# Kernel tuning notes

Measured on AMD Instinct MI355X. Metric: run time of the kernel, lower is better.

Reference implementation:

```python
import jax, jax.numpy as jnp
import numpy as np

B, T, D, M = 4, 4096, 2048, 512


def setup_inputs() -> dict:
    key = jax.random.key(0)
    ks = jax.random.split(key, 6)
    x = jax.random.normal(ks[0], (B, T, D), dtype=jnp.float32)
    memory_state = jnp.zeros((B, M), dtype=jnp.float32)
    # xavier_normal-style init for the linear layers, zero biases
    Wv = jax.random.normal(ks[1], (M, D), dtype=jnp.float32) * np.float32(np.sqrt(2.0 / (D + M)))
    bv = jnp.zeros((M,), dtype=jnp.float32)
    Wg = jax.random.normal(ks[2], (D, D + M), dtype=jnp.float32) * np.float32(np.sqrt(2.0 / (2 * D + M)))
    bg = jnp.zeros((D,), dtype=jnp.float32)
    time_decay = jax.random.normal(ks[3], (M,), dtype=jnp.float32) * 0.01
    time_first = jax.random.normal(ks[4], (M,), dtype=jnp.float32) * 0.01
    return dict(x=x, memory_state=memory_state, Wv=Wv, bv=bv, Wg=Wg, bg=bg,
                time_decay=time_decay, time_first=time_first)


def reference(x, memory_state, Wv, bv, Wg, bg, time_decay, time_first):
    # v = value_proj(x): [B, T, M]
    v = jnp.einsum('btd,md->btm', x, Wv) + bv
    decay = jax.nn.sigmoid(time_decay) * 0.9 + 0.1   # [M]
    first = jax.nn.sigmoid(time_first)               # [M]

    # Recurrence: s_0 = memory_state; wv_t = v_t + s_t*first; s_{t+1} = s_t*decay + v_t
    def step(s, v_t):
        wv_t = v_t + s * first
        return s * decay + v_t, wv_t

    v_tb = jnp.swapaxes(v, 0, 1)                     # [T, B, M] for scan over time
    next_memory, wv_tb = jax.lax.scan(step, memory_state, v_tb)
    weighted_values = jnp.swapaxes(wv_tb, 0, 1)      # [B, T, M]

    # output = x + output_gate(concat[x, weighted_values])
    combined = jnp.concatenate([x, weighted_values], axis=-1)  # [B, T, D+M]
    output = x + jnp.einsum('btk,dk->btd', combined, Wg) + bg
    return output, next_memory
```

## Files before the change

### kernel.cpp

```cpp
#include <hip/hip_runtime.h>
#include <hip/hip_bf16.h>
#include <stdint.h>

#define BB 4
#define TT 4096
#define DDIM 2048
#define MDIM 512
#define NROWS (BB * TT)
#define KCAT (DDIM + MDIM)
#define CHUNK 64
#define NCH (TT / CHUNK)

typedef __attribute__((ext_vector_type(8))) short bf16x8;
typedef __attribute__((ext_vector_type(4))) float f32x4;

#define WAITVM(N) asm volatile("s_waitcnt vmcnt(" #N ")" ::: "memory")
#define SBAR()    asm volatile("s_barrier" ::: "memory")

__device__ __forceinline__ unsigned short f2bf(float f) {
  unsigned u = __float_as_uint(f);
  return (unsigned short)((u + 0x7fffu + ((u >> 16) & 1u)) >> 16);
}
__device__ __forceinline__ float sigm(float x) { return 1.0f / (1.0f + expf(-x)); }

__device__ __forceinline__ void gload16(const void* g, void* l) {
  __builtin_amdgcn_global_load_lds(
      (const __attribute__((address_space(1))) unsigned int*)g,
      (__attribute__((address_space(3))) unsigned int*)l, 16, 0, 0);
}

__global__ void cvt_x_kernel(const float* __restrict__ x, unsigned short* __restrict__ comb) {
  size_t i = (size_t)blockIdx.x * 256 + threadIdx.x;
  size_t row = i >> 9;
  size_t c = (i & 511) << 2;
  float4 f = ((const float4*)x)[i];
  ushort4 o;
  o.x = f2bf(f.x); o.y = f2bf(f.y); o.z = f2bf(f.z); o.w = f2bf(f.w);
  *((ushort4*)(comb + row * KCAT + c)) = o;
}

__global__ void cvt_w_kernel(const float* __restrict__ src, unsigned short* __restrict__ dst, long n4) {
  long i = (long)blockIdx.x * 256 + threadIdx.x;
  if (i >= n4) return;
  float4 f = ((const float4*)src)[i];
  ushort4 o;
  o.x = f2bf(f.x); o.y = f2bf(f.y); o.z = f2bf(f.z); o.w = f2bf(f.w);
  ((ushort4*)dst)[i] = o;
}

template<int EPI>
__global__ __launch_bounds__(256, 3) void gemm_bf16_kernel(
    const unsigned short* __restrict__ A, long lda,
    const unsigned short* __restrict__ B, long K,
    float* __restrict__ out, long ldo,
    const float* __restrict__ bias,
    const float* __restrict__ xres,
    int ncb)
{
  __shared__ __align__(16) unsigned char ldsA[3][8192];
  __shared__ __align__(16) unsigned char ldsB[3][8192];

  const int tid = threadIdx.x;
  const int nwg = gridDim.x;
  int lin = blockIdx.x;
  lin = (lin & 7) * (nwg >> 3) + (lin >> 3);
  const long row0 = (long)(lin / ncb) * 128;
  const long col0 = (long)(lin % ncb) * 128;

  const int lane = tid & 63;
  const int wave = tid >> 6;
  const int wr = (wave >> 1) * 64;
  const int wc = (wave & 1) * 64;

  const int srow = tid >> 2;
  const int skq = ((tid & 3) ^ ((tid >> 3) & 3)) * 8;
  const unsigned short* aS = A + (row0 + srow) * lda + skq;
  const unsigned short* bS = B + (col0 + srow) * K + skq;
  const int ldst = tid * 16;

  f32x4 acc[4][4];
#pragma unroll
  for (int i = 0; i < 4; ++i)
#pragma unroll
    for (int j = 0; j < 4; ++j)
      acc[i][j] = {0.f, 0.f, 0.f, 0.f};

  int aOff[4], bOff[4];
#pragma unroll
  for (int i = 0; i < 4; ++i) {
    const int ra = wr + i * 16 + (lane & 15);
    const int rb = wc + i * 16 + (lane & 15);
    aOff[i] = ra * 64 + ((((lane >> 4) ^ ((ra >> 1) & 3))) << 4);
    bOff[i] = rb * 64 + ((((lane >> 4) ^ ((rb >> 1) & 3))) << 4);
  }

  const int nt = (int)(K >> 5);

  auto STAGE = [&](int buf, int t) {
    const long koff = (long)t << 5;
#pragma unroll
    for (int j = 0; j < 2; ++j) {
      gload16(aS + koff + (long)j * 64 * lda, &ldsA[buf][j * 4096 + ldst]);
      gload16(bS + koff + (long)j * 64 * K, &ldsB[buf][j * 4096 + ldst]);
    }
  };

  auto COMPUTE = [&](int cb) {
    bf16x8 af[4], bfr[4];
#pragma unroll
    for (int i = 0; i < 4; ++i) af[i] = *(const bf16x8*)(&ldsA[cb][aOff[i]]);
#pragma unroll
    for (int i = 0; i < 4; ++i) bfr[i] = *(const bf16x8*)(&ldsB[cb][bOff[i]]);
    __builtin_amdgcn_s_setprio(1);
#pragma unroll
    for (int i = 0; i < 4; ++i)
#pragma unroll
      for (int j = 0; j < 4; ++j)
        acc[i][j] = __builtin_amdgcn_mfma_f32_16x16x32_bf16(af[i], bfr[j], acc[i][j], 0, 0, 0);
    __builtin_amdgcn_s_setprio(0);
  };

  STAGE(0, 0);
  STAGE(1, 1);
  int cur = 0, stg = 2;
  for (int t = 0; t < nt - 2; ++t) {
    WAITVM(4);
    SBAR();
    STAGE(stg, t + 2);
    COMPUTE(cur);
    cur = (cur == 2) ? 0 : cur + 1;
    stg = (stg == 2) ? 0 : stg + 1;
  }
  WAITVM(4);
  SBAR();
  COMPUTE(cur);
  cur = (cur == 2) ? 0 : cur + 1;
  WAITVM(0);
  SBAR();
  COMPUTE(cur);

  const int orow = (lane >> 4) * 4;
  const int ocol = lane & 15;
#pragma unroll
  for (int i = 0; i < 4; ++i) {
    const long gr0 = row0 + wr + i * 16 + orow;
#pragma unroll
    for (int j = 0; j < 4; ++j) {
      const long gc = col0 + wc + j * 16 + ocol;
      const float bb = bias[gc];
#pragma unroll
      for (int r = 0; r < 4; ++r) {
        const long gr = gr0 + r;
        float v = acc[i][j][r] + bb;
        if (EPI == 1) v += xres[gr * ldo + gc];
        out[gr * ldo + gc] = v;
      }
    }
  }
}

__global__ void scan_local_kernel(const float* __restrict__ v, float* __restrict__ s_loc,
                                  const float* __restrict__ td) {
  const int m = threadIdx.x;
  const int c = blockIdx.x;
  const int b = blockIdx.y;
  const float decay = sigm(td[m]) * 0.9f + 0.1f;
  const float* vp = v + ((size_t)b * TT + (size_t)c * CHUNK) * MDIM + m;
  float s = 0.f;
#pragma unroll 8
  for (int t = 0; t < CHUNK; ++t) s = s * decay + vp[(size_t)t * MDIM];
  s_loc[((size_t)b * NCH + c) * MDIM + m] = s;
}

__global__ void scan_chunks_kernel(const float* __restrict__ s_loc, const float* __restrict__ mem0,
                                   float* __restrict__ s_in, float* __restrict__ nextmem,
                                   const float* __restrict__ td) {
  const int m = threadIdx.x;
  const int b = blockIdx.x;
  const float decay = sigm(td[m]) * 0.9f + 0.1f;
  const float d2 = decay * decay, d4 = d2 * d2, d8 = d4 * d4;
  const float d16 = d8 * d8, d32 = d16 * d16, dL = d32 * d32;
  float s = mem0[(size_t)b * MDIM + m];
  for (int c = 0; c < NCH; ++c) {
    const size_t idx = ((size_t)b * NCH + c) * MDIM + m;
    s_in[idx] = s;
    s = s * dL + s_loc[idx];
  }
  nextmem[(size_t)b * MDIM + m] = s;
}

__global__ void scan_replay_kernel(const float* __restrict__ v, const float* __restrict__ s_in,
                                   unsigned short* __restrict__ comb,
                                   const float* __restrict__ td, const float* __restrict__ tf) {
  const int m = threadIdx.x;
  const int c = blockIdx.x;
  const int b = blockIdx.y;
  const float decay = sigm(td[m]) * 0.9f + 0.1f;
  const float first = sigm(tf[m]);
  float s = s_in[((size_t)b * NCH + c) * MDIM + m];
  const float* vp = v + ((size_t)b * TT + (size_t)c * CHUNK) * MDIM + m;
  unsigned short* wp = comb + ((size_t)b * TT + (size_t)c * CHUNK) * KCAT + DDIM + m;
#pragma unroll 4
  for (int t = 0; t < CHUNK; ++t) {
    const float vv = vp[(size_t)t * MDIM];
    wp[(size_t)t * KCAT] = f2bf(vv + s * first);
    s = s * decay + vv;
  }
}

extern "C" void kernel_launch(void* const* d_in, const int* in_sizes, int n_in,
                              void* d_out, int out_size, void* d_ws, size_t ws_size,
                              hipStream_t stream) {
  const float* x    = (const float*)d_in[0];
  const float* mem0 = (const float*)d_in[1];
  const float* Wv   = (const float*)d_in[2];
  const float* bv   = (const float*)d_in[3];
  const float* Wg   = (const float*)d_in[4];
  const float* bg   = (const float*)d_in[5];
  const float* td   = (const float*)d_in[6];
  const float* tf   = (const float*)d_in[7];

  float* out = (float*)d_out;
  float* nextmem = out + (size_t)NROWS * DDIM;
  float* vbuf = out;

  unsigned short* comb = (unsigned short*)d_ws;
  unsigned short* WvB  = comb + (size_t)NROWS * KCAT;
  unsigned short* WgB  = WvB + (size_t)MDIM * DDIM;
  float* s_loc = (float*)(WgB + (size_t)DDIM * KCAT);
  float* s_in  = s_loc + (size_t)BB * NCH * MDIM;

  cvt_x_kernel<<<(NROWS * DDIM / 4) / 256, 256, 0, stream>>>(x, comb);
  cvt_w_kernel<<<(MDIM * DDIM / 4) / 256, 256, 0, stream>>>(Wv, WvB, (long)MDIM * DDIM / 4);
  cvt_w_kernel<<<(DDIM * KCAT / 4) / 256, 256, 0, stream>>>(Wg, WgB, (long)DDIM * KCAT / 4);

  gemm_bf16_kernel<0><<<(NROWS / 128) * (MDIM / 128), 256, 0, stream>>>(
      comb, KCAT, WvB, DDIM, vbuf, MDIM, bv, nullptr, MDIM / 128);

  scan_local_kernel<<<dim3(NCH, BB), MDIM, 0, stream>>>(vbuf, s_loc, td);
  scan_chunks_kernel<<<BB, MDIM, 0, stream>>>(s_loc, mem0, s_in, nextmem, td);
  scan_replay_kernel<<<dim3(NCH, BB), MDIM, 0, stream>>>(vbuf, s_in, comb, td, tf);

  gemm_bf16_kernel<1><<<(NROWS / 128) * (DDIM / 128), 256, 0, stream>>>(
      comb, KCAT, WgB, KCAT, out, DDIM, bg, x, DDIM / 128);
}
```

Baseline: 552.2 us.

## Use 256x256-tile, 8-wave GEMM for output gate with bf16 residual

```diff
diff --git a/kernel.cpp b/kernel.cpp
--- a/kernel.cpp
+++ b/kernel.cpp
@@ -153,6 +153,128 @@
         const long gr = gr0 + r;
         float v = acc[i][j][r] + bb;
         if (EPI == 1) v += xres[gr * ldo + gc];
+        out[gr * ldo + gc] = v;
+      }
+    }
+  }
+}
+
+template<int RESID>
+__global__ __launch_bounds__(512, 2) void gemm256_kernel(
+    const unsigned short* __restrict__ A, long lda,
+    const unsigned short* __restrict__ B, long K,
+    float* __restrict__ out, long ldo,
+    const float* __restrict__ bias,
+    int ncb)
+{
+  __shared__ __align__(16) unsigned char ldsA[3][16384];
+  __shared__ __align__(16) unsigned char ldsB[3][16384];
+
+  const int tid = threadIdx.x;
+  const int nwg = gridDim.x;
+  int lin = blockIdx.x;
+  lin = (lin & 7) * (nwg >> 3) + (lin >> 3);
+  const long row0 = (long)(lin / ncb) * 256;
+  const long col0 = (long)(lin % ncb) * 256;
+
+  const int lane = tid & 63;
+  const int wave = tid >> 6;
+  const int wr = (wave >> 2) * 128;
+  const int wc = (wave & 3) * 64;
+
+  const int srow = tid >> 2;
+  const int skq = ((tid & 3) ^ ((tid >> 2) & 3)) * 8;
+  const unsigned short* aS = A + (row0 + srow) * lda + skq;
+  const unsigned short* bS = B + (col0 + srow) * K + skq;
+  const int ldst = tid * 16;
+
+  f32x4 acc[8][4];
+#pragma unroll
+  for (int i = 0; i < 8; ++i)
+#pragma unroll
+    for (int j = 0; j < 4; ++j)
+      acc[i][j] = {0.f, 0.f, 0.f, 0.f};
+
+  const int slotb = ((lane >> 4) ^ (lane & 3)) << 4;
+  int aOff[8], bOff[4];
+#pragma unroll
+  for (int h = 0; h < 2; ++h)
+#pragma unroll
+    for (int ii = 0; ii < 4; ++ii)
+      aOff[h * 4 + ii] = (wr + h * 64 + ii * 16 + (lane & 15)) * 64 + slotb;
+#pragma unroll
+  for (int jj = 0; jj < 4; ++jj)
+    bOff[jj] = (wc + jj * 16 + (lane & 15)) * 64 + slotb;
+
+  const int nt = (int)(K >> 5);
+
+  auto STAGE_A = [&](int buf, int t) {
+    const long koff = (long)t << 5;
+#pragma unroll
+    for (int j = 0; j < 2; ++j)
+      gload16(aS + koff + (long)j * 128 * lda, &ldsA[buf][j * 8192 + ldst]);
+  };
+  auto STAGE_B = [&](int buf, int t) {
+    const long koff = (long)t << 5;
+#pragma unroll
+    for (int j = 0; j < 2; ++j)
+      gload16(bS + koff + (long)j * 128 * K, &ldsB[buf][j * 8192 + ldst]);
+  };
+
+  STAGE_A(0, 0); STAGE_B(0, 0);
+  STAGE_A(1, 1); STAGE_B(1, 1);
+  int cur = 0, stg = 2;
+  for (int t = 0; t < nt; ++t) {
+    if (t < nt - 1) { WAITVM(4); } else { WAITVM(0); }
+    SBAR();
+    const bool doStage = (t + 2 < nt);
+    bf16x8 bfr[4], af[4];
+#pragma unroll
+    for (int jj = 0; jj < 4; ++jj) bfr[jj] = *(const bf16x8*)(&ldsB[cur][bOff[jj]]);
+#pragma unroll
+    for (int ii = 0; ii < 4; ++ii) af[ii] = *(const bf16x8*)(&ldsA[cur][aOff[ii]]);
+    if (doStage) STAGE_A(stg, t + 2);
+    SBAR();
+    __builtin_amdgcn_s_setprio(1);
+#pragma unroll
+    for (int ii = 0; ii < 4; ++ii)
+#pragma unroll
+      for (int jj = 0; jj < 4; ++jj)
+        acc[ii][jj] = __builtin_amdgcn_mfma_f32_16x16x32_bf16(af[ii], bfr[jj], acc[ii][jj], 0, 0, 0);
+    __builtin_amdgcn_s_setprio(0);
+    SBAR();
+#pragma unroll
+    for (int ii = 0; ii < 4; ++ii) af[ii] = *(const bf16x8*)(&ldsA[cur][aOff[4 + ii]]);
+    if (doStage) STAGE_B(stg, t + 2);
+    SBAR();
+    __builtin_amdgcn_s_setprio(1);
+#pragma unroll
+    for (int ii = 0; ii < 4; ++ii)
+#pragma unroll
+      for (int jj = 0; jj < 4; ++jj)
+        acc[4 + ii][jj] = __builtin_amdgcn_mfma_f32_16x16x32_bf16(af[ii], bfr[jj], acc[4 + ii][jj], 0, 0, 0);
+    __builtin_amdgcn_s_setprio(0);
+    cur = (cur == 2) ? 0 : cur + 1;
+    stg = (stg == 2) ? 0 : stg + 1;
+  }
+
+  const int orow = (lane >> 4) * 4;
+  const int ocol = lane & 15;
+#pragma unroll
+  for (int i = 0; i < 8; ++i) {
+    const long gr0 = row0 + wr + i * 16 + orow;
+#pragma unroll
+    for (int j = 0; j < 4; ++j) {
+      const long gc = col0 + wc + j * 16 + ocol;
+      const float bb = bias[gc];
+#pragma unroll
+      for (int r = 0; r < 4; ++r) {
+        const long gr = gr0 + r;
+        float v = acc[i][j][r] + bb;
+        if (RESID == 1) {
+          unsigned short us = A[gr * lda + gc];
+          v += __uint_as_float(((unsigned)us) << 16);
+        }
         out[gr * ldo + gc] = v;
       }
     }
@@ -241,6 +363,6 @@
   scan_chunks_kernel<<<BB, MDIM, 0, stream>>>(s_loc, mem0, s_in, nextmem, td);
   scan_replay_kernel<<<dim3(NCH, BB), MDIM, 0, stream>>>(vbuf, s_in, comb, td, tf);
 
-  gemm_bf16_kernel<1><<<(NROWS / 128) * (DDIM / 128), 256, 0, stream>>>(
-      comb, KCAT, WgB, KCAT, out, DDIM, bg, x, DDIM / 128);
-}
+  gemm256_kernel<1><<<(NROWS / 256) * (DDIM / 256), 512, 0, stream>>>(
+      comb, KCAT, WgB, KCAT, out, DDIM, bg, DDIM / 256);
+}
```

Measured after the change: 491.0 us. 1.12x faster.
